# Kernel tuning notes

Measured on AMD Instinct MI355X. Metric: run time of the kernel, lower is better.

## Reference

```python
import jax, jax.numpy as jnp
import numpy as np

B, L, F, T = 512, 512, 128, 512

def setup_inputs() -> dict:
    key = jax.random.key(0)
    ks = jax.random.split(key, 8)
    s_ih = 1.0 / np.sqrt(L)
    return {
        "h0": jax.random.normal(ks[0], (1, B, L), jnp.float32),
        "c0": jax.random.normal(ks[1], (1, B, L), jnp.float32),
        "W_ih": jax.random.normal(ks[2], (4 * L, F), jnp.float32) * s_ih,
        "W_hh": jax.random.normal(ks[3], (4 * L, L), jnp.float32) * s_ih,
        "b_ih": jax.random.normal(ks[4], (4 * L,), jnp.float32) * s_ih,
        "b_hh": jax.random.normal(ks[5], (4 * L,), jnp.float32) * s_ih,
        "W_dense": jax.random.normal(ks[6], (F, L), jnp.float32) * s_ih,
        "b_dense": jax.random.normal(ks[7], (F,), jnp.float32) * s_ih,
        "seq_len": T,
    }

def reference(h0, c0, W_ih, W_hh, b_ih, b_hh, W_dense, b_dense, seq_len):
    h = h0[0]  # [B, L] (squeeze num_layers dim)
    c = c0[0]
    x = h @ W_dense.T + b_dense  # initial x_i = dense(h)

    def step(carry, _):
        x, h, c = carry
        gates = x @ W_ih.T + b_ih + h @ W_hh.T + b_hh  # [B, 4L]
        i, f, g, o = jnp.split(gates, 4, axis=-1)
        c2 = jax.nn.sigmoid(f) * c + jax.nn.sigmoid(i) * jnp.tanh(g)
        h2 = jax.nn.sigmoid(o) * jnp.tanh(c2)
        x2 = h2 @ W_dense.T + b_dense  # [B, F]
        return (x2, h2, c2), x2

    _, xs = jax.lax.scan(step, (x, h, c), None, length=seq_len)  # xs: [T, B, F]
    # torch code cats along axis=1 then views (-1, seq_len, n_features) -> [B, T, F]
    return jnp.transpose(xs, (1, 0, 2))
```

## Files before the change

kernel.cpp:

```cpp
#include <hip/hip_runtime.h>
#include <hip/hip_fp16.h>

#define T_STEPS 512
#define BDIM 512
#define LDIM 512
#define FDIM 128

typedef _Float16 half8 __attribute__((ext_vector_type(8)));
typedef float f4_t __attribute__((ext_vector_type(4)));

#define OFF_WPERM   0u
#define OFF_WDH     2097152u
#define OFF_BCOMB   2228224u
#define OFF_HBUF0   2236416u
#define OFF_HBUF1   2760704u
#define OFF_FLAGS   3284992u

__device__ __forceinline__ float sigmoidf_(float x) { return 1.f / (1.f + __expf(-x)); }
__device__ __forceinline__ float tanhf_(float x) { return 1.f - 2.f / (__expf(2.f * x) + 1.f); }

__device__ __forceinline__ void gload_lds16(const void* g, void* l) {
    __builtin_amdgcn_global_load_lds(
        (const __attribute__((address_space(1))) void*)g,
        (__attribute__((address_space(3))) void*)l, 16, 0, 0);
}

__device__ __forceinline__ unsigned long long aload64(const void* p) {
    return __hip_atomic_load((unsigned long long*)p, __ATOMIC_RELAXED, __HIP_MEMORY_SCOPE_AGENT);
}
__device__ __forceinline__ unsigned aload32(const void* p) {
    return __hip_atomic_load((unsigned*)p, __ATOMIC_RELAXED, __HIP_MEMORY_SCOPE_AGENT);
}
__device__ __forceinline__ void astore32(void* p, unsigned v) {
    __hip_atomic_store((unsigned*)p, v, __ATOMIC_RELAXED, __HIP_MEMORY_SCOPE_AGENT);
}

__global__ __launch_bounds__(256) void k_prep_w(
    const float* __restrict__ W_ih, const float* __restrict__ W_hh,
    const float* __restrict__ b_ih, const float* __restrict__ b_hh,
    const float* __restrict__ W_dense, const float* __restrict__ b_dense,
    _Float16* __restrict__ Wperm, float* __restrict__ bcomb)
{
    __shared__ float ih[FDIM];
    const int pr = blockIdx.x;
    const int gate = pr & 3, sg = pr >> 2;
    const int j = gate * 512 + sg;
    const int tid = threadIdx.x;
    if (tid < FDIM) ih[tid] = W_ih[j * FDIM + tid];
    __syncthreads();
    const int k0 = tid * 2;
    float a0 = W_hh[(size_t)j * LDIM + k0];
    float a1 = W_hh[(size_t)j * LDIM + k0 + 1];
    for (int f = 0; f < FDIM; ++f) {
        const float w = ih[f];
        a0 += w * W_dense[f * LDIM + k0];
        a1 += w * W_dense[f * LDIM + k0 + 1];
    }
    const int s = (pr & 7) << 3;
    Wperm[(size_t)pr * LDIM + (k0 ^ s)] = (_Float16)a0;
    Wperm[(size_t)pr * LDIM + (k0 ^ s) + 1] = (_Float16)a1;
    if (tid == 0) {
        float acc = b_ih[j] + b_hh[j];
        for (int f = 0; f < FDIM; ++f) acc += ih[f] * b_dense[f];
        bcomb[j] = acc;
    }
}

__global__ __launch_bounds__(256) void k_prep_misc(
    const float* __restrict__ W_dense, const float* __restrict__ h0,
    _Float16* __restrict__ Wdh, _Float16* __restrict__ hbuf0)
{
    const int bid = blockIdx.x, tid = threadIdx.x;
    const int k0 = tid * 2;
    if (bid < FDIM) {
        const int f = bid; const int s = (f & 7) << 3;
        Wdh[f * LDIM + (k0 ^ s)] = (_Float16)W_dense[f * LDIM + k0];
        Wdh[f * LDIM + (k0 ^ s) + 1] = (_Float16)W_dense[f * LDIM + k0 + 1];
    } else {
        const int r = bid - FDIM; const int s = (r & 7) << 3;
        hbuf0[r * LDIM + (k0 ^ s)] = (_Float16)h0[r * LDIM + k0];
        hbuf0[r * LDIM + (k0 ^ s) + 1] = (_Float16)h0[r * LDIM + k0 + 1];
    }
}

#define LDS_W   0
#define LDS_WD  65536
#define LDS_H   69632
#define LDS_TOT 135168

__device__ __forceinline__ void stage_h(char* smem, const char* gh, int tid) {
    #pragma unroll
    for (int ch = 0; ch < 4; ++ch) {
        unsigned long long tmp[8];
        #pragma unroll
        for (int r = 0; r < 8; ++r) tmp[r] = aload64(gh + ((ch * 8 + r) * 256 + tid) * 8);
        #pragma unroll
        for (int r = 0; r < 8; ++r)
            *(unsigned long long*)(smem + LDS_H + ((ch * 8 + r) * 256 + tid) * 8) = tmp[r];
    }
}

__global__ __launch_bounds__(256, 1) void k_persist(
    const _Float16* __restrict__ Wperm, const _Float16* __restrict__ Wdh,
    const float* __restrict__ bcomb, const float* __restrict__ bdense,
    const float* __restrict__ c0,
    _Float16* __restrict__ hb0, _Float16* __restrict__ hb1,
    float* __restrict__ out, unsigned* __restrict__ flags)
{
    __shared__ __align__(16) char smem[LDS_TOT];
    const int cb = blockIdx.x;
    const int g = blockIdx.y;
    const int tid = threadIdx.x;
    const int w = tid >> 6, lane = tid & 63;
    const int wm = w >> 1, wn = w & 1;
    const int lr = lane & 15, lh = lane >> 4;

    {
        const char* gw = (const char*)Wperm + (size_t)cb * 65536;
        #pragma unroll
        for (int i = 0; i < 16; ++i)
            gload_lds16(gw + (i * 256 + tid) * 16, smem + LDS_W + (i * 256 + tid) * 16);
        const char* gd = (const char*)Wdh + (size_t)cb * 4096;
        gload_lds16(gd + tid * 16, smem + LDS_WD + tid * 16);
    }

    float bi[2], bf[2], bg[2], bo[2];
    float creg[2][2];
    #pragma unroll
    for (int mt2 = 0; mt2 < 2; ++mt2) {
        const int sg = cb * 16 + 8 * wm + 4 * mt2 + lh;
        bi[mt2] = bcomb[0 * 512 + sg];
        bf[mt2] = bcomb[1 * 512 + sg];
        bg[mt2] = bcomb[2 * 512 + sg];
        bo[mt2] = bcomb[3 * 512 + sg];
        #pragma unroll
        for (int nt2 = 0; nt2 < 2; ++nt2) {
            const int row = g * 64 + (2 * wn + nt2) * 16 + lr;
            creg[mt2][nt2] = c0[(size_t)row * LDIM + sg];
        }
    }
    float bd[4];
    #pragma unroll
    for (int j = 0; j < 4; ++j) bd[j] = bdense[cb * 4 + j];

    const int ntx = 2 * wn + wm;
    const int swA = (lr & 7) << 4;
    const int swD = ((cb * 4 + lr) & 7) << 4;
    const char* pA0 = smem + LDS_W + ((2 * wm + 0) * 16 + lr) * 1024;
    const char* pA1 = smem + LDS_W + ((2 * wm + 1) * 16 + lr) * 1024;
    const char* pB0 = smem + LDS_H + ((2 * wn + 0) * 16 + lr) * 1024;
    const char* pB1 = smem + LDS_H + ((2 * wn + 1) * 16 + lr) * 1024;
    const char* pBx = smem + LDS_H + (ntx * 16 + lr) * 1024;
    const char* pD  = smem + LDS_WD + lr * 1024;

    unsigned* myflags = flags + g * 32;

    stage_h(smem, (const char*)hb0 + (size_t)g * 65536, tid);
    __syncthreads();

    for (int t = 1; t <= T_STEPS; ++t) {
        char* hout = (char*)((t & 1) ? hb1 : hb0);

        f4_t acc[2][2] = {};
        #pragma unroll
        for (int kt = 0; kt < 16; ++kt) {
            const int kb = kt * 64 + lh * 16;
            const half8 a0 = *(const half8*)(pA0 + (kb ^ swA));
            const half8 a1 = *(const half8*)(pA1 + (kb ^ swA));
            const half8 b0 = *(const half8*)(pB0 + (kb ^ swA));
            const half8 b1 = *(const half8*)(pB1 + (kb ^ swA));
            acc[0][0] = __builtin_amdgcn_mfma_f32_16x16x32_f16(a0, b0, acc[0][0], 0, 0, 0);
            acc[0][1] = __builtin_amdgcn_mfma_f32_16x16x32_f16(a0, b1, acc[0][1], 0, 0, 0);
            acc[1][0] = __builtin_amdgcn_mfma_f32_16x16x32_f16(a1, b0, acc[1][0], 0, 0, 0);
            acc[1][1] = __builtin_amdgcn_mfma_f32_16x16x32_f16(a1, b1, acc[1][1], 0, 0, 0);
        }

        #pragma unroll
        for (int mt2 = 0; mt2 < 2; ++mt2) {
            const int sg = cb * 16 + 8 * wm + 4 * mt2 + lh;
            #pragma unroll
            for (int nt2 = 0; nt2 < 2; ++nt2) {
                const int row = g * 64 + (2 * wn + nt2) * 16 + lr;
                const float iv = sigmoidf_(acc[mt2][nt2][0] + bi[mt2]);
                const float fv = sigmoidf_(acc[mt2][nt2][1] + bf[mt2]);
                const float gv = tanhf_(acc[mt2][nt2][2] + bg[mt2]);
                const float ov = sigmoidf_(acc[mt2][nt2][3] + bo[mt2]);
                const float cnew = fv * creg[mt2][nt2] + iv * gv;
                const float hnew = ov * tanhf_(cnew);
                creg[mt2][nt2] = cnew;
                const unsigned u = (unsigned)__builtin_bit_cast(unsigned short, (_Float16)hnew);
                const unsigned up = (unsigned)__shfl_xor((int)u, 16);
                if ((lh & 1) == 0) {
                    const unsigned word = u | (up << 16);
                    astore32(hout + row * 1024 + (sg ^ ((row & 7) << 3)) * 2, word);
                }
            }
        }

        f4_t accx = {};
        if (t >= 2) {
            #pragma unroll
            for (int kt = 0; kt < 16; ++kt) {
                const int kb = kt * 64 + lh * 16;
                const half8 ad = *(const half8*)(pD + (kb ^ swD));
                const half8 b = *(const half8*)(pBx + (kb ^ swA));
                accx = __builtin_amdgcn_mfma_f32_16x16x32_f16(ad, b, accx, 0, 0, 0);
            }
        }

        __syncthreads();
        if (tid == 0) astore32(myflags + cb, (unsigned)t);

        if (t >= 2 && lh == 0) {
            const int row = g * 64 + ntx * 16 + lr;
            float* o = &out[((size_t)row * T_STEPS + (t - 2)) * FDIM + cb * 4];
            o[0] = accx[0] + bd[0];
            o[1] = accx[1] + bd[1];
            o[2] = accx[2] + bd[2];
            o[3] = accx[3] + bd[3];
        }

        if (w == 0) {
            for (;;) {
                const unsigned v = (lane < 32) ? aload32(myflags + lane) : 0xffffffffu;
                if (__all(v >= (unsigned)t)) break;
                __builtin_amdgcn_s_sleep(1);
            }
        }
        __syncthreads();

        stage_h(smem, (const char*)((t & 1) ? hb1 : hb0) + (size_t)g * 65536, tid);
        __syncthreads();
    }

    {
        f4_t accx = {};
        #pragma unroll
        for (int kt = 0; kt < 16; ++kt) {
            const int kb = kt * 64 + lh * 16;
            const half8 ad = *(const half8*)(pD + (kb ^ swD));
            const half8 b = *(const half8*)(pBx + (kb ^ swA));
            accx = __builtin_amdgcn_mfma_f32_16x16x32_f16(ad, b, accx, 0, 0, 0);
        }
        if (lh == 0) {
            const int row = g * 64 + ntx * 16 + lr;
            float* o = &out[((size_t)row * T_STEPS + (T_STEPS - 1)) * FDIM + cb * 4];
            o[0] = accx[0] + bd[0];
            o[1] = accx[1] + bd[1];
            o[2] = accx[2] + bd[2];
            o[3] = accx[3] + bd[3];
        }
    }
}

extern "C" void kernel_launch(void* const* d_in, const int* in_sizes, int n_in,
                              void* d_out, int out_size, void* d_ws, size_t ws_size,
                              hipStream_t stream)
{
    const float* h0      = (const float*)d_in[0];
    const float* c0      = (const float*)d_in[1];
    const float* W_ih    = (const float*)d_in[2];
    const float* W_hh    = (const float*)d_in[3];
    const float* b_ih    = (const float*)d_in[4];
    const float* b_hh    = (const float*)d_in[5];
    const float* W_dense = (const float*)d_in[6];
    const float* b_dense = (const float*)d_in[7];
    float* out = (float*)d_out;
    char* ws = (char*)d_ws;

    _Float16* Wperm = (_Float16*)(ws + OFF_WPERM);
    _Float16* Wdh   = (_Float16*)(ws + OFF_WDH);
    float*    bcomb = (float*)(ws + OFF_BCOMB);
    _Float16* hb0   = (_Float16*)(ws + OFF_HBUF0);
    _Float16* hb1   = (_Float16*)(ws + OFF_HBUF1);
    unsigned* flags = (unsigned*)(ws + OFF_FLAGS);

    hipMemsetAsync(flags, 0, 1024, stream);
    k_prep_w<<<2048, 256, 0, stream>>>(W_ih, W_hh, b_ih, b_hh, W_dense, b_dense, Wperm, bcomb);
    k_prep_misc<<<FDIM + BDIM, 256, 0, stream>>>(W_dense, h0, Wdh, hb0);
    k_persist<<<dim3(32, 8), 256, 0, stream>>>(Wperm, Wdh, bcomb, b_dense, c0, hb0, hb1, out, flags);
}
```

Baseline: 2.812 ms.

## Hold weight fragments in registers and fuse dense-output MFMA into gate loop

Loads the per-wave fragments of the combined recurrent weights and the dense weights from LDS into registers once before the time loop, so each step reads only h from LDS. The dense-output MFMA is folded into the gate GEMM loop and reuses the h fragments already loaded, instead of running as a second K loop. The XOR swizzle granularity moves from 16-byte to 128-byte chunks to match the new access pattern. This costs many extra VGPRs (48 half8 fragments per lane), which may lower occupancy or cause spills. At t=1 the fused MFMA computes an extra, unused dense output.

New measurement: 2.838 ms. No clear change (+0.9%).

```diff
diff --git a/kernel.cpp b/kernel.cpp
--- a/kernel.cpp
+++ b/kernel.cpp
@@ -56,7 +56,7 @@
         a0 += w * W_dense[f * LDIM + k0];
         a1 += w * W_dense[f * LDIM + k0 + 1];
     }
-    const int s = (pr & 7) << 3;
+    const int s = (pr & 7) << 6;
     Wperm[(size_t)pr * LDIM + (k0 ^ s)] = (_Float16)a0;
     Wperm[(size_t)pr * LDIM + (k0 ^ s) + 1] = (_Float16)a1;
     if (tid == 0) {
@@ -73,11 +73,11 @@
     const int bid = blockIdx.x, tid = threadIdx.x;
     const int k0 = tid * 2;
     if (bid < FDIM) {
-        const int f = bid; const int s = (f & 7) << 3;
+        const int f = bid; const int s = (f & 7) << 6;
         Wdh[f * LDIM + (k0 ^ s)] = (_Float16)W_dense[f * LDIM + k0];
         Wdh[f * LDIM + (k0 ^ s) + 1] = (_Float16)W_dense[f * LDIM + k0 + 1];
     } else {
-        const int r = bid - FDIM; const int s = (r & 7) << 3;
+        const int r = bid - FDIM; const int s = (r & 7) << 6;
         hbuf0[r * LDIM + (k0 ^ s)] = (_Float16)h0[r * LDIM + k0];
         hbuf0[r * LDIM + (k0 ^ s) + 1] = (_Float16)h0[r * LDIM + k0 + 1];
     }
@@ -144,8 +144,8 @@
     for (int j = 0; j < 4; ++j) bd[j] = bdense[cb * 4 + j];
 
     const int ntx = 2 * wn + wm;
-    const int swA = (lr & 7) << 4;
-    const int swD = ((cb * 4 + lr) & 7) << 4;
+    const int swz = (lr & 7) << 7;
+    const int swD = ((cb * 4 + lr) & 7) << 7;
     const char* pA0 = smem + LDS_W + ((2 * wm + 0) * 16 + lr) * 1024;
     const char* pA1 = smem + LDS_W + ((2 * wm + 1) * 16 + lr) * 1024;
     const char* pB0 = smem + LDS_H + ((2 * wn + 0) * 16 + lr) * 1024;
@@ -158,21 +158,30 @@
     stage_h(smem, (const char*)hb0 + (size_t)g * 65536, tid);
     __syncthreads();
 
+    half8 aA0[16], aA1[16], aD[16];
+    #pragma unroll
+    for (int kt = 0; kt < 16; ++kt) {
+        const int kb = kt * 64 + lh * 16;
+        aA0[kt] = *(const half8*)(pA0 + (kb ^ swz));
+        aA1[kt] = *(const half8*)(pA1 + (kb ^ swz));
+        aD[kt]  = *(const half8*)(pD  + (kb ^ swD));
+    }
+
     for (int t = 1; t <= T_STEPS; ++t) {
         char* hout = (char*)((t & 1) ? hb1 : hb0);
 
         f4_t acc[2][2] = {};
+        f4_t accx = {};
         #pragma unroll
         for (int kt = 0; kt < 16; ++kt) {
             const int kb = kt * 64 + lh * 16;
-            const half8 a0 = *(const half8*)(pA0 + (kb ^ swA));
-            const half8 a1 = *(const half8*)(pA1 + (kb ^ swA));
-            const half8 b0 = *(const half8*)(pB0 + (kb ^ swA));
-            const half8 b1 = *(const half8*)(pB1 + (kb ^ swA));
-            acc[0][0] = __builtin_amdgcn_mfma_f32_16x16x32_f16(a0, b0, acc[0][0], 0, 0, 0);
-            acc[0][1] = __builtin_amdgcn_mfma_f32_16x16x32_f16(a0, b1, acc[0][1], 0, 0, 0);
-            acc[1][0] = __builtin_amdgcn_mfma_f32_16x16x32_f16(a1, b0, acc[1][0], 0, 0, 0);
-            acc[1][1] = __builtin_amdgcn_mfma_f32_16x16x32_f16(a1, b1, acc[1][1], 0, 0, 0);
+            const half8 b0 = *(const half8*)(pB0 + (kb ^ swz));
+            const half8 b1 = *(const half8*)(pB1 + (kb ^ swz));
+            acc[0][0] = __builtin_amdgcn_mfma_f32_16x16x32_f16(aA0[kt], b0, acc[0][0], 0, 0, 0);
+            acc[0][1] = __builtin_amdgcn_mfma_f32_16x16x32_f16(aA0[kt], b1, acc[0][1], 0, 0, 0);
+            acc[1][0] = __builtin_amdgcn_mfma_f32_16x16x32_f16(aA1[kt], b0, acc[1][0], 0, 0, 0);
+            acc[1][1] = __builtin_amdgcn_mfma_f32_16x16x32_f16(aA1[kt], b1, acc[1][1], 0, 0, 0);
+            accx = __builtin_amdgcn_mfma_f32_16x16x32_f16(aD[kt], wm ? b1 : b0, accx, 0, 0, 0);
         }
 
         #pragma unroll
@@ -192,19 +201,8 @@
                 const unsigned up = (unsigned)__shfl_xor((int)u, 16);
                 if ((lh & 1) == 0) {
                     const unsigned word = u | (up << 16);
-                    astore32(hout + row * 1024 + (sg ^ ((row & 7) << 3)) * 2, word);
+                    astore32(hout + row * 1024 + ((sg * 2) ^ ((row & 7) << 7)), word);
                 }
-            }
-        }
-
-        f4_t accx = {};
-        if (t >= 2) {
-            #pragma unroll
-            for (int kt = 0; kt < 16; ++kt) {
-                const int kb = kt * 64 + lh * 16;
-                const half8 ad = *(const half8*)(pD + (kb ^ swD));
-                const half8 b = *(const half8*)(pBx + (kb ^ swA));
-                accx = __builtin_amdgcn_mfma_f32_16x16x32_f16(ad, b, accx, 0, 0, 0);
             }
         }
 
@@ -238,9 +236,8 @@
         #pragma unroll
         for (int kt = 0; kt < 16; ++kt) {
             const int kb = kt * 64 + lh * 16;
-            const half8 ad = *(const half8*)(pD + (kb ^ swD));
-            const half8 b = *(const half8*)(pBx + (kb ^ swA));
-            accx = __builtin_amdgcn_mfma_f32_16x16x32_f16(ad, b, accx, 0, 0, 0);
+            const half8 b = *(const half8*)(pBx + (kb ^ swz));
+            accx = __builtin_amdgcn_mfma_f32_16x16x32_f16(aD[kt], b, accx, 0, 0, 0);
         }
         if (lh == 0) {
             const int row = g * 64 + ntx * 16 + lr;
```
